# Kernel optimization log

Measured on AMD Instinct MI355X. Metric: run time of the kernel, lower is better.

Reference implementation:

```python
import jax, jax.numpy as jnp
import numpy as np

D_IN, D_HID, D_OUT = 256, 256, 10  # mlp dims (init_kwargs)


def mlp(params, x):
    # x: [D_IN] (single sample, matching fnet_single's unsqueeze/squeeze)
    h = jnp.tanh(x @ params["W1"] + params["b1"])
    h = jnp.tanh(h @ params["W2"] + params["b2"])
    return h @ params["W3"] + params["b3"]  # [D_OUT]


def setup_inputs() -> dict:
    key = jax.random.key(0)
    ks = jax.random.split(key, 8)
    rn = lambda k, shp, scale: (jax.random.normal(k, shp, jnp.float32) * scale)
    return {
        "x1": jax.random.normal(ks[0], (64, D_IN), jnp.float32),
        "x2": jax.random.normal(ks[1], (64, D_IN), jnp.float32),
        "W1": rn(ks[2], (D_IN, D_HID), 1.0 / np.sqrt(D_IN)),
        "b1": jnp.zeros((D_HID,), jnp.float32),
        "W2": rn(ks[3], (D_HID, D_HID), 1.0 / np.sqrt(D_HID)),
        "b2": jnp.zeros((D_HID,), jnp.float32),
        "W3": rn(ks[4], (D_HID, D_OUT), 1.0 / np.sqrt(D_HID)),
        "b3": jnp.zeros((D_OUT,), jnp.float32),
    }


def reference(x1, x2, W1, b1, W2, b2, W3, b3):
    params = {"W1": W1, "b1": b1, "W2": W2, "b2": b2, "W3": W3, "b3": b3}
    # vmap(jacrev(fnet_single), (None, 0)): per-sample Jacobian w.r.t. every param tensor
    jac_fn = jax.vmap(jax.jacrev(mlp, argnums=0), in_axes=(None, 0))
    jac1 = jax.tree_util.tree_leaves(jac_fn(params, x1))  # list of [N, O, *pshape]
    jac2 = jax.tree_util.tree_leaves(jac_fn(params, x2))  # list of [M, O, *pshape]
    # flatten(2): [N, O, f] per param tensor
    j1 = [j.reshape(j.shape[0], j.shape[1], -1) for j in jac1]
    j2 = [j.reshape(j.shape[0], j.shape[1], -1) for j in jac2]
    # per-param einsum, then sum over param tensors (== stack(...).sum(0))
    result = sum(jnp.einsum("Naf,Mbf->NMab", a, b) for a, b in zip(j1, j2))
    return result  # [N, M, O, O]
```

## Files before the change

### kernel.cpp

```cpp
#include <hip/hip_runtime.h>

#define NS 64
#define D  256
#define O  10
#define TK 64
#define LSTR 68

__global__ __launch_bounds__(512) void prep1_kernel(
    const float* __restrict__ x1, const float* __restrict__ x2,
    const float* __restrict__ W1, const float* __restrict__ b1,
    const float* __restrict__ W2, const float* __restrict__ b2,
    const float* __restrict__ W3,
    float* __restrict__ h1o, float* __restrict__ S1o,
    float* __restrict__ h2o, float* __restrict__ G2L,
    float* __restrict__ W2T)
{
    int t = threadIdx.x;
    if (blockIdx.x >= 128) {
        int blk = blockIdx.x - 128;
        int bxT = blk & 7, byT = blk >> 3;
        __shared__ float tile[32][33];
        int txT = t & 31, tyT = t >> 5;
        #pragma unroll
        for (int r = 0; r < 2; ++r)
            tile[tyT + 16 * r][txT] = W2[(byT * 32 + tyT + 16 * r) * D + bxT * 32 + txT];
        __syncthreads();
        #pragma unroll
        for (int r = 0; r < 2; ++r)
            W2T[(bxT * 32 + tyT + 16 * r) * D + byT * 32 + txT] = tile[txT][tyT + 16 * r];
        return;
    }

    int s = blockIdx.x;
    const float* x = (s < NS) ? (x1 + s * D) : (x2 + (s - NS) * D);
    int tt = t & 255, half = t >> 8;
    int k0 = half * 128;
    __shared__ float xs[D];
    __shared__ float hs[D];
    __shared__ float part[2][D];

    if (half == 0) xs[tt] = x[tt];
    __syncthreads();

    float acc = half ? 0.0f : b1[tt];
    #pragma unroll 8
    for (int k = 0; k < 128; ++k) acc = fmaf(xs[k0 + k], W1[(k0 + k) * D + tt], acc);
    part[half][tt] = acc;
    __syncthreads();

    if (half == 0) {
        float h1v = tanhf(part[0][tt] + part[1][tt]);
        h1o[s * D + tt] = h1v;
        S1o[s * D + tt] = 1.0f - h1v * h1v;
        hs[tt] = h1v;
    }
    __syncthreads();

    acc = half ? 0.0f : b2[tt];
    #pragma unroll 8
    for (int k = 0; k < 128; ++k) acc = fmaf(hs[k0 + k], W2[(k0 + k) * D + tt], acc);
    part[half][tt] = acc;
    __syncthreads();

    if (half == 0) {
        float h2v = tanhf(part[0][tt] + part[1][tt]);
        h2o[s * D + tt] = h2v;
        hs[tt] = 1.0f - h2v * h2v;
    }
    __syncthreads();

    for (int idx = t; idx < O * D; idx += 512) {
        int a = idx >> 8, i = idx & 255;
        G2L[(s * O + a) * D + i] = hs[i] * W3[i * O + a];
    }
}

__global__ __launch_bounds__(512) void prep2_kernel(
    const float* __restrict__ W2T, const float* __restrict__ S1,
    const float* __restrict__ G2L, float* __restrict__ G1L,
    const float* __restrict__ x1, const float* __restrict__ x2,
    const float* __restrict__ h1, const float* __restrict__ h2,
    float* __restrict__ dots)
{
    int t = threadIdx.x;
    if (blockIdx.x < 128) {
        int s = blockIdx.x;
        __shared__ float g2s[O * D];
        __shared__ float red[O * D];
        for (int idx = t; idx < D * O; idx += 512) g2s[idx] = G2L[s * D * O + idx];
        __syncthreads();

        int tt = t & 255, half = t >> 8;
        int j0 = half * 128;
        float acc[O];
        #pragma unroll
        for (int a = 0; a < O; ++a) acc[a] = 0.0f;
        #pragma unroll 8
        for (int j = 0; j < 128; ++j) {
            float w = W2T[(j0 + j) * D + tt];
            #pragma unroll
            for (int a = 0; a < O; ++a) acc[a] = fmaf(w, g2s[a * D + j0 + j], acc[a]);
        }
        if (half == 1) {
            #pragma unroll
            for (int a = 0; a < O; ++a) red[a * D + tt] = acc[a];
        }
        __syncthreads();
        if (half == 0) {
            float s1 = S1[s * D + tt];
            #pragma unroll
            for (int a = 0; a < O; ++a)
                G1L[(s * O + a) * D + tt] = s1 * (acc[a] + red[a * D + tt]);
        }
        return;
    }

    int idx = blockIdx.x - 128;
    int which = idx >> 6, n = idx & 63;
    const float* A; const float* B;
    if (which == 0)      { A = x1 + n * D; B = x2; }
    else if (which == 1) { A = h1 + n * D; B = h1 + NS * D; }
    else                 { A = h2 + n * D; B = h2 + NS * D; }
    __shared__ float as[D];
    if (t < D) as[t] = A[t];
    __syncthreads();
    int wave = t >> 6, lane = t & 63;
    for (int m = wave; m < NS; m += 8) {
        const float* Bv = B + m * D;
        float v = as[lane] * Bv[lane]
                + as[64 + lane] * Bv[64 + lane]
                + as[128 + lane] * Bv[128 + lane]
                + as[192 + lane] * Bv[192 + lane];
        #pragma unroll
        for (int off = 32; off > 0; off >>= 1) v += __shfl_xor(v, off);
        if (lane == 0) dots[(which * NS + n) * NS + m] = v;
    }
}

__global__ __launch_bounds__(256) void ntk_gemm_kernel(
    const float* __restrict__ G1L, const float* __restrict__ G2L,
    const float* __restrict__ dots, float* __restrict__ out)
{
    int by = blockIdx.x / 20, bx = blockIdx.x % 20;
    __shared__ float A1[32 * LSTR], B1[32 * LSTR], A2[32 * LSTR], B2[32 * LSTR];
    int t = threadIdx.x;
    int tx = t & 15, ty = t >> 4;

    float acc1[2][2], acc2[2][2];
    #pragma unroll
    for (int i = 0; i < 2; ++i)
        #pragma unroll
        for (int j = 0; j < 2; ++j) { acc1[i][j] = 0.0f; acc2[i][j] = 0.0f; }

    const float* arow1 = G1L + (by * 32) * D;
    const float* brow1 = G1L + (640 + bx * 32) * D;
    const float* arow2 = G2L + (by * 32) * D;
    const float* brow2 = G2L + (640 + bx * 32) * D;

    for (int kc = 0; kc < D; kc += TK) {
        __syncthreads();
        #pragma unroll
        for (int u = 0; u < 2; ++u) {
            int idx = t + u * 256;
            int r = idx >> 4, c4 = idx & 15;
            int goff = r * D + kc + c4 * 4;
            int loff = r * LSTR + c4 * 4;
            *(float4*)&A1[loff] = *(const float4*)&arow1[goff];
            *(float4*)&B1[loff] = *(const float4*)&brow1[goff];
            *(float4*)&A2[loff] = *(const float4*)&arow2[goff];
            *(float4*)&B2[loff] = *(const float4*)&brow2[goff];
        }
        __syncthreads();
        #pragma unroll
        for (int kk = 0; kk < TK; kk += 4) {
            float4 a1[2], b1v[2], a2[2], b2v[2];
            #pragma unroll
            for (int i = 0; i < 2; ++i) {
                a1[i] = *(const float4*)&A1[(2 * ty + i) * LSTR + kk];
                a2[i] = *(const float4*)&A2[(2 * ty + i) * LSTR + kk];
            }
            #pragma unroll
            for (int j = 0; j < 2; ++j) {
                b1v[j] = *(const float4*)&B1[(tx + 16 * j) * LSTR + kk];
                b2v[j] = *(const float4*)&B2[(tx + 16 * j) * LSTR + kk];
            }
            #pragma unroll
            for (int i = 0; i < 2; ++i)
                #pragma unroll
                for (int j = 0; j < 2; ++j) {
                    acc1[i][j] = fmaf(a1[i].x, b1v[j].x, acc1[i][j]);
                    acc1[i][j] = fmaf(a1[i].y, b1v[j].y, acc1[i][j]);
                    acc1[i][j] = fmaf(a1[i].z, b1v[j].z, acc1[i][j]);
                    acc1[i][j] = fmaf(a1[i].w, b1v[j].w, acc1[i][j]);
                    acc2[i][j] = fmaf(a2[i].x, b2v[j].x, acc2[i][j]);
                    acc2[i][j] = fmaf(a2[i].y, b2v[j].y, acc2[i][j]);
                    acc2[i][j] = fmaf(a2[i].z, b2v[j].z, acc2[i][j]);
                    acc2[i][j] = fmaf(a2[i].w, b2v[j].w, acc2[i][j]);
                }
        }
    }

    #pragma unroll
    for (int i = 0; i < 2; ++i) {
        int R = by * 32 + 2 * ty + i;
        int n = R / 10, a = R - n * 10;
        #pragma unroll
        for (int j = 0; j < 2; ++j) {
            int C = bx * 32 + tx + 16 * j;
            int m = C / 10, b = C - m * 10;
            float cx  = 1.0f + dots[0 * NS * NS + n * NS + m];
            float ch1 = 1.0f + dots[1 * NS * NS + n * NS + m];
            float val = cx * acc1[i][j] + ch1 * acc2[i][j];
            if (a == b) val += 1.0f + dots[2 * NS * NS + n * NS + m];
            out[(n * NS + m) * (O * O) + a * O + b] = val;
        }
    }
}

extern "C" void kernel_launch(void* const* d_in, const int* in_sizes, int n_in,
                              void* d_out, int out_size, void* d_ws, size_t ws_size,
                              hipStream_t stream) {
    const float* x1 = (const float*)d_in[0];
    const float* x2 = (const float*)d_in[1];
    const float* W1 = (const float*)d_in[2];
    const float* b1 = (const float*)d_in[3];
    const float* W2 = (const float*)d_in[4];
    const float* b2 = (const float*)d_in[5];
    const float* W3 = (const float*)d_in[6];

    float* ws   = (float*)d_ws;
    float* h1   = ws;
    float* S1   = h1 + 128 * D;
    float* h2   = S1 + 128 * D;
    float* G2L  = h2 + 128 * D;
    float* G1L  = G2L + 1280 * D;
    float* W2T  = G1L + 1280 * D;
    float* dots = W2T + D * D;
    float* out  = (float*)d_out;

    hipLaunchKernelGGL(prep1_kernel, dim3(192), dim3(512), 0, stream,
                       x1, x2, W1, b1, W2, b2, W3, h1, S1, h2, G2L, W2T);
    hipLaunchKernelGGL(prep2_kernel, dim3(320), dim3(512), 0, stream,
                       W2T, S1, G2L, G1L, x1, x2, h1, h2, dots);
    hipLaunchKernelGGL(ntk_gemm_kernel, dim3(400), dim3(256), 0, stream,
                       G1L, G2L, dots, out);
}
```

Measured before the change: 125.0 us.

## Split-K the NTK GEMM with 64x64 tiles and a separate combine kernel

The GEMM moves from 32x32 output tiles over the full K=256 to 64x64 tiles with a 4x4 register micro-tile, split into four K-slices of 64, keeping 400 blocks. Each block writes raw partial products to a new workspace region. A new combine kernel sums the four partials, applies the dot-product scaling and the diagonal term, and writes the output. This aims to raise arithmetic intensity per block, at the cost of an extra launch and roughly 13 MB of partial-sum traffic written and re-read, plus a larger workspace requirement.

Result: faster. 115.8 us (-7.3%).

```diff
diff --git a/kernel.cpp b/kernel.cpp
--- a/kernel.cpp
+++ b/kernel.cpp
@@ -3,8 +3,8 @@
 #define NS 64
 #define D  256
 #define O  10
-#define TK 64
-#define LSTR 68
+#define TK 32
+#define LSTR 36
 
 __global__ __launch_bounds__(512) void prep1_kernel(
     const float* __restrict__ x1, const float* __restrict__ x2,
@@ -139,30 +139,32 @@
 
 __global__ __launch_bounds__(256) void ntk_gemm_kernel(
     const float* __restrict__ G1L, const float* __restrict__ G2L,
-    const float* __restrict__ dots, float* __restrict__ out)
-{
-    int by = blockIdx.x / 20, bx = blockIdx.x % 20;
-    __shared__ float A1[32 * LSTR], B1[32 * LSTR], A2[32 * LSTR], B2[32 * LSTR];
+    float* __restrict__ P1p, float* __restrict__ P2p)
+{
+    int tile = blockIdx.x % 100;
+    int ks   = blockIdx.x / 100;
+    int by = tile / 10, bx = tile % 10;
+    __shared__ float A1[64 * LSTR], B1[64 * LSTR], A2[64 * LSTR], B2[64 * LSTR];
     int t = threadIdx.x;
     int tx = t & 15, ty = t >> 4;
 
-    float acc1[2][2], acc2[2][2];
+    float acc1[4][4], acc2[4][4];
     #pragma unroll
-    for (int i = 0; i < 2; ++i)
-        #pragma unroll
-        for (int j = 0; j < 2; ++j) { acc1[i][j] = 0.0f; acc2[i][j] = 0.0f; }
-
-    const float* arow1 = G1L + (by * 32) * D;
-    const float* brow1 = G1L + (640 + bx * 32) * D;
-    const float* arow2 = G2L + (by * 32) * D;
-    const float* brow2 = G2L + (640 + bx * 32) * D;
-
-    for (int kc = 0; kc < D; kc += TK) {
+    for (int i = 0; i < 4; ++i)
+        #pragma unroll
+        for (int j = 0; j < 4; ++j) { acc1[i][j] = 0.0f; acc2[i][j] = 0.0f; }
+
+    const float* arow1 = G1L + (by * 64) * D + ks * 64;
+    const float* brow1 = G1L + (640 + bx * 64) * D + ks * 64;
+    const float* arow2 = G2L + (by * 64) * D + ks * 64;
+    const float* brow2 = G2L + (640 + bx * 64) * D + ks * 64;
+
+    for (int kc = 0; kc < 64; kc += TK) {
         __syncthreads();
         #pragma unroll
         for (int u = 0; u < 2; ++u) {
             int idx = t + u * 256;
-            int r = idx >> 4, c4 = idx & 15;
+            int r = idx >> 3, c4 = idx & 7;
             int goff = r * D + kc + c4 * 4;
             int loff = r * LSTR + c4 * 4;
             *(float4*)&A1[loff] = *(const float4*)&arow1[goff];
@@ -173,21 +175,21 @@
         __syncthreads();
         #pragma unroll
         for (int kk = 0; kk < TK; kk += 4) {
-            float4 a1[2], b1v[2], a2[2], b2v[2];
-            #pragma unroll
-            for (int i = 0; i < 2; ++i) {
-                a1[i] = *(const float4*)&A1[(2 * ty + i) * LSTR + kk];
-                a2[i] = *(const float4*)&A2[(2 * ty + i) * LSTR + kk];
+            float4 a1[4], b1v[4], a2[4], b2v[4];
+            #pragma unroll
+            for (int i = 0; i < 4; ++i) {
+                a1[i] = *(const float4*)&A1[(4 * ty + i) * LSTR + kk];
+                a2[i] = *(const float4*)&A2[(4 * ty + i) * LSTR + kk];
             }
             #pragma unroll
-            for (int j = 0; j < 2; ++j) {
+            for (int j = 0; j < 4; ++j) {
                 b1v[j] = *(const float4*)&B1[(tx + 16 * j) * LSTR + kk];
                 b2v[j] = *(const float4*)&B2[(tx + 16 * j) * LSTR + kk];
             }
             #pragma unroll
-            for (int i = 0; i < 2; ++i)
+            for (int i = 0; i < 4; ++i)
                 #pragma unroll
-                for (int j = 0; j < 2; ++j) {
+                for (int j = 0; j < 4; ++j) {
                     acc1[i][j] = fmaf(a1[i].x, b1v[j].x, acc1[i][j]);
                     acc1[i][j] = fmaf(a1[i].y, b1v[j].y, acc1[i][j]);
                     acc1[i][j] = fmaf(a1[i].z, b1v[j].z, acc1[i][j]);
@@ -201,19 +203,41 @@
     }
 
     #pragma unroll
-    for (int i = 0; i < 2; ++i) {
-        int R = by * 32 + 2 * ty + i;
+    for (int i = 0; i < 4; ++i) {
+        int R = by * 64 + 4 * ty + i;
+        float* p1row = P1p + (ks * 640 + R) * 640;
+        float* p2row = P2p + (ks * 640 + R) * 640;
+        #pragma unroll
+        for (int j = 0; j < 4; ++j) {
+            int C = bx * 64 + tx + 16 * j;
+            p1row[C] = acc1[i][j];
+            p2row[C] = acc2[i][j];
+        }
+    }
+}
+
+__global__ __launch_bounds__(256) void combine_kernel(
+    const float* __restrict__ P1p, const float* __restrict__ P2p,
+    const float* __restrict__ dots, float* __restrict__ out)
+{
+    int base = blockIdx.x * 1024;
+    #pragma unroll
+    for (int u = 0; u < 4; ++u) {
+        int e = base + u * 256 + threadIdx.x;
+        int R = e / 640, C = e - R * 640;
+        float p1 = 0.0f, p2 = 0.0f;
+        #pragma unroll
+        for (int s = 0; s < 4; ++s) {
+            p1 += P1p[(s * 640 + R) * 640 + C];
+            p2 += P2p[(s * 640 + R) * 640 + C];
+        }
         int n = R / 10, a = R - n * 10;
-        #pragma unroll
-        for (int j = 0; j < 2; ++j) {
-            int C = bx * 32 + tx + 16 * j;
-            int m = C / 10, b = C - m * 10;
-            float cx  = 1.0f + dots[0 * NS * NS + n * NS + m];
-            float ch1 = 1.0f + dots[1 * NS * NS + n * NS + m];
-            float val = cx * acc1[i][j] + ch1 * acc2[i][j];
-            if (a == b) val += 1.0f + dots[2 * NS * NS + n * NS + m];
-            out[(n * NS + m) * (O * O) + a * O + b] = val;
-        }
+        int m = C / 10, b = C - m * 10;
+        float cx  = 1.0f + dots[0 * NS * NS + n * NS + m];
+        float ch1 = 1.0f + dots[1 * NS * NS + n * NS + m];
+        float val = cx * p1 + ch1 * p2;
+        if (a == b) val += 1.0f + dots[2 * NS * NS + n * NS + m];
+        out[(n * NS + m) * (O * O) + a * O + b] = val;
     }
 }
 
@@ -236,6 +260,8 @@
     float* G1L  = G2L + 1280 * D;
     float* W2T  = G1L + 1280 * D;
     float* dots = W2T + D * D;
+    float* P1p  = dots + 3 * NS * NS;
+    float* P2p  = P1p + 4 * 640 * 640;
     float* out  = (float*)d_out;
 
     hipLaunchKernelGGL(prep1_kernel, dim3(192), dim3(512), 0, stream,
@@ -243,5 +269,7 @@
     hipLaunchKernelGGL(prep2_kernel, dim3(320), dim3(512), 0, stream,
                        W2T, S1, G2L, G1L, x1, x2, h1, h2, dots);
     hipLaunchKernelGGL(ntk_gemm_kernel, dim3(400), dim3(256), 0, stream,
-                       G1L, G2L, dots, out);
-}
+                       G1L, G2L, P1p, P2p);
+    hipLaunchKernelGGL(combine_kernel, dim3(400), dim3(256), 0, stream,
+                       P1p, P2p, dots, out);
+}
```

## Store Jacobian factors as bf16 and compute NTK GEMM with MFMA

Applied to the files above, without the earlier changes.

G1/G2 Jacobian factor matrices are rounded to bf16 when written. The final 640x640x256 contractions move from an LDS-tiled fp32 FMA kernel to single-wave blocks issuing 16x16x32 bf16 MFMA instructions straight from global memory. prep2's W2 back-projection loop also reads four k values per step with float4 LDS loads. This cuts memory traffic and ALU work, but adds bf16 rounding error to the result and drops LDS reuse in the GEMM.

Measured after the change: 101.5 us, median of 2. -18.8%, faster.

```diff
diff --git a/kernel.cpp b/kernel.cpp
--- a/kernel.cpp
+++ b/kernel.cpp
@@ -3,8 +3,20 @@
 #define NS 64
 #define D  256
 #define O  10
-#define TK 64
-#define LSTR 68
+
+typedef unsigned short u16;
+typedef __attribute__((ext_vector_type(8))) short bf16x8;
+typedef __attribute__((ext_vector_type(4))) float f32x4;
+
+__device__ __forceinline__ u16 f2bf(float f) {
+    union { float f; unsigned u; } v; v.f = f;
+    unsigned r = v.u + 0x7FFFu + ((v.u >> 16) & 1u);
+    return (u16)(r >> 16);
+}
+__device__ __forceinline__ float bf2f(u16 h) {
+    union { unsigned u; float f; } v; v.u = ((unsigned)h) << 16;
+    return v.f;
+}
 
 __global__ __launch_bounds__(512) void prep1_kernel(
     const float* __restrict__ x1, const float* __restrict__ x2,
@@ -12,7 +24,7 @@
     const float* __restrict__ W2, const float* __restrict__ b2,
     const float* __restrict__ W3,
     float* __restrict__ h1o, float* __restrict__ S1o,
-    float* __restrict__ h2o, float* __restrict__ G2L,
+    float* __restrict__ h2o, u16* __restrict__ G2b,
     float* __restrict__ W2T)
 {
     int t = threadIdx.x;
@@ -71,13 +83,13 @@
 
     for (int idx = t; idx < O * D; idx += 512) {
         int a = idx >> 8, i = idx & 255;
-        G2L[(s * O + a) * D + i] = hs[i] * W3[i * O + a];
+        G2b[(s * O + a) * D + i] = f2bf(hs[i] * W3[i * O + a]);
     }
 }
 
 __global__ __launch_bounds__(512) void prep2_kernel(
     const float* __restrict__ W2T, const float* __restrict__ S1,
-    const float* __restrict__ G2L, float* __restrict__ G1L,
+    const u16* __restrict__ G2b, u16* __restrict__ G1b,
     const float* __restrict__ x1, const float* __restrict__ x2,
     const float* __restrict__ h1, const float* __restrict__ h2,
     float* __restrict__ dots)
@@ -87,7 +99,7 @@
         int s = blockIdx.x;
         __shared__ float g2s[O * D];
         __shared__ float red[O * D];
-        for (int idx = t; idx < D * O; idx += 512) g2s[idx] = G2L[s * D * O + idx];
+        for (int idx = t; idx < D * O; idx += 512) g2s[idx] = bf2f(G2b[s * D * O + idx]);
         __syncthreads();
 
         int tt = t & 255, half = t >> 8;
@@ -95,11 +107,20 @@
         float acc[O];
         #pragma unroll
         for (int a = 0; a < O; ++a) acc[a] = 0.0f;
-        #pragma unroll 8
-        for (int j = 0; j < 128; ++j) {
-            float w = W2T[(j0 + j) * D + tt];
+        #pragma unroll 2
+        for (int j = 0; j < 128; j += 4) {
+            float w0 = W2T[(j0 + j + 0) * D + tt];
+            float w1 = W2T[(j0 + j + 1) * D + tt];
+            float w2 = W2T[(j0 + j + 2) * D + tt];
+            float w3 = W2T[(j0 + j + 3) * D + tt];
             #pragma unroll
-            for (int a = 0; a < O; ++a) acc[a] = fmaf(w, g2s[a * D + j0 + j], acc[a]);
+            for (int a = 0; a < O; ++a) {
+                float4 g = *(const float4*)&g2s[a * D + j0 + j];
+                acc[a] = fmaf(w0, g.x, acc[a]);
+                acc[a] = fmaf(w1, g.y, acc[a]);
+                acc[a] = fmaf(w2, g.z, acc[a]);
+                acc[a] = fmaf(w3, g.w, acc[a]);
+            }
         }
         if (half == 1) {
             #pragma unroll
@@ -110,7 +131,7 @@
             float s1 = S1[s * D + tt];
             #pragma unroll
             for (int a = 0; a < O; ++a)
-                G1L[(s * O + a) * D + tt] = s1 * (acc[a] + red[a * D + tt]);
+                G1b[(s * O + a) * D + tt] = f2bf(s1 * (acc[a] + red[a * D + tt]));
         }
         return;
     }
@@ -137,83 +158,43 @@
     }
 }
 
-__global__ __launch_bounds__(256) void ntk_gemm_kernel(
-    const float* __restrict__ G1L, const float* __restrict__ G2L,
+__global__ __launch_bounds__(64) void ntk_mfma_kernel(
+    const u16* __restrict__ G1b, const u16* __restrict__ G2b,
     const float* __restrict__ dots, float* __restrict__ out)
 {
-    int by = blockIdx.x / 20, bx = blockIdx.x % 20;
-    __shared__ float A1[32 * LSTR], B1[32 * LSTR], A2[32 * LSTR], B2[32 * LSTR];
-    int t = threadIdx.x;
-    int tx = t & 15, ty = t >> 4;
-
-    float acc1[2][2], acc2[2][2];
+    int lane = threadIdx.x;
+    int by = blockIdx.x / 40, bx = blockIdx.x % 40;
+    int R0 = by * 16, C0 = bx * 16;
+    int lm = lane & 15;
+    int lk = (lane >> 4) * 8;
+
+    const u16* a1p = G1b + (R0 + lm) * D + lk;
+    const u16* b1p = G1b + (640 + C0 + lm) * D + lk;
+    const u16* a2p = G2b + (R0 + lm) * D + lk;
+    const u16* b2p = G2b + (640 + C0 + lm) * D + lk;
+
+    f32x4 acc1 = {0.f, 0.f, 0.f, 0.f}, acc2 = {0.f, 0.f, 0.f, 0.f};
     #pragma unroll
-    for (int i = 0; i < 2; ++i)
-        #pragma unroll
-        for (int j = 0; j < 2; ++j) { acc1[i][j] = 0.0f; acc2[i][j] = 0.0f; }
-
-    const float* arow1 = G1L + (by * 32) * D;
-    const float* brow1 = G1L + (640 + bx * 32) * D;
-    const float* arow2 = G2L + (by * 32) * D;
-    const float* brow2 = G2L + (640 + bx * 32) * D;
-
-    for (int kc = 0; kc < D; kc += TK) {
-        __syncthreads();
-        #pragma unroll
-        for (int u = 0; u < 2; ++u) {
-            int idx = t + u * 256;
-            int r = idx >> 4, c4 = idx & 15;
-            int goff = r * D + kc + c4 * 4;
-            int loff = r * LSTR + c4 * 4;
-            *(float4*)&A1[loff] = *(const float4*)&arow1[goff];
-            *(float4*)&B1[loff] = *(const float4*)&brow1[goff];
-            *(float4*)&A2[loff] = *(const float4*)&arow2[goff];
-            *(float4*)&B2[loff] = *(const float4*)&brow2[goff];
-        }
-        __syncthreads();
-        #pragma unroll
-        for (int kk = 0; kk < TK; kk += 4) {
-            float4 a1[2], b1v[2], a2[2], b2v[2];
-            #pragma unroll
-            for (int i = 0; i < 2; ++i) {
-                a1[i] = *(const float4*)&A1[(2 * ty + i) * LSTR + kk];
-                a2[i] = *(const float4*)&A2[(2 * ty + i) * LSTR + kk];
-            }
-            #pragma unroll
-            for (int j = 0; j < 2; ++j) {
-                b1v[j] = *(const float4*)&B1[(tx + 16 * j) * LSTR + kk];
-                b2v[j] = *(const float4*)&B2[(tx + 16 * j) * LSTR + kk];
-            }
-            #pragma unroll
-            for (int i = 0; i < 2; ++i)
-                #pragma unroll
-                for (int j = 0; j < 2; ++j) {
-                    acc1[i][j] = fmaf(a1[i].x, b1v[j].x, acc1[i][j]);
-                    acc1[i][j] = fmaf(a1[i].y, b1v[j].y, acc1[i][j]);
-                    acc1[i][j] = fmaf(a1[i].z, b1v[j].z, acc1[i][j]);
-                    acc1[i][j] = fmaf(a1[i].w, b1v[j].w, acc1[i][j]);
-                    acc2[i][j] = fmaf(a2[i].x, b2v[j].x, acc2[i][j]);
-                    acc2[i][j] = fmaf(a2[i].y, b2v[j].y, acc2[i][j]);
-                    acc2[i][j] = fmaf(a2[i].z, b2v[j].z, acc2[i][j]);
-                    acc2[i][j] = fmaf(a2[i].w, b2v[j].w, acc2[i][j]);
-                }
-        }
-    }
-
+    for (int ks = 0; ks < 8; ++ks) {
+        bf16x8 a1 = *(const bf16x8*)(a1p + ks * 32);
+        bf16x8 b1 = *(const bf16x8*)(b1p + ks * 32);
+        bf16x8 a2 = *(const bf16x8*)(a2p + ks * 32);
+        bf16x8 b2 = *(const bf16x8*)(b2p + ks * 32);
+        acc1 = __builtin_amdgcn_mfma_f32_16x16x32_bf16(a1, b1, acc1, 0, 0, 0);
+        acc2 = __builtin_amdgcn_mfma_f32_16x16x32_bf16(a2, b2, acc2, 0, 0, 0);
+    }
+
+    int C = C0 + lm;
+    int m = C / 10, b = C - m * 10;
     #pragma unroll
-    for (int i = 0; i < 2; ++i) {
-        int R = by * 32 + 2 * ty + i;
+    for (int r = 0; r < 4; ++r) {
+        int R = R0 + (lane >> 4) * 4 + r;
         int n = R / 10, a = R - n * 10;
-        #pragma unroll
-        for (int j = 0; j < 2; ++j) {
-            int C = bx * 32 + tx + 16 * j;
-            int m = C / 10, b = C - m * 10;
-            float cx  = 1.0f + dots[0 * NS * NS + n * NS + m];
-            float ch1 = 1.0f + dots[1 * NS * NS + n * NS + m];
-            float val = cx * acc1[i][j] + ch1 * acc2[i][j];
-            if (a == b) val += 1.0f + dots[2 * NS * NS + n * NS + m];
-            out[(n * NS + m) * (O * O) + a * O + b] = val;
-        }
+        float cx  = 1.0f + dots[0 * NS * NS + n * NS + m];
+        float ch1 = 1.0f + dots[1 * NS * NS + n * NS + m];
+        float val = cx * acc1[r] + ch1 * acc2[r];
+        if (a == b) val += 1.0f + dots[2 * NS * NS + n * NS + m];
+        out[(n * NS + m) * (O * O) + a * O + b] = val;
     }
 }
 
@@ -232,16 +213,16 @@
     float* h1   = ws;
     float* S1   = h1 + 128 * D;
     float* h2   = S1 + 128 * D;
-    float* G2L  = h2 + 128 * D;
-    float* G1L  = G2L + 1280 * D;
-    float* W2T  = G1L + 1280 * D;
+    float* W2T  = h2 + 128 * D;
     float* dots = W2T + D * D;
+    u16*  G2b   = (u16*)(dots + 3 * NS * NS);
+    u16*  G1b   = G2b + 1280 * D;
     float* out  = (float*)d_out;
 
     hipLaunchKernelGGL(prep1_kernel, dim3(192), dim3(512), 0, stream,
-                       x1, x2, W1, b1, W2, b2, W3, h1, S1, h2, G2L, W2T);
+                       x1, x2, W1, b1, W2, b2, W3, h1, S1, h2, G2b, W2T);
     hipLaunchKernelGGL(prep2_kernel, dim3(320), dim3(512), 0, stream,
-                       W2T, S1, G2L, G1L, x1, x2, h1, h2, dots);
-    hipLaunchKernelGGL(ntk_gemm_kernel, dim3(400), dim3(256), 0, stream,
-                       G1L, G2L, dots, out);
-}
+                       W2T, S1, G2b, G1b, x1, x2, h1, h2, dots);
+    hipLaunchKernelGGL(ntk_mfma_kernel, dim3(1600), dim3(64), 0, stream,
+                       G1b, G2b, dots, out);
+}
```
